# Kernel optimization log

Hardware: AMD Instinct MI355X
Metric: run time of the kernel (lower is better)

## Reference

```python
import jax, jax.numpy as jnp
import numpy as np

N, D, K = 8192, 64, 32

def setup_inputs() -> dict:
    key = jax.random.key(0)
    anchor_x = jax.random.normal(key, (N, D), dtype=jnp.float32)
    return {"anchor_x": anchor_x, "k": K}

def reference(anchor_x, k):
    """Equivalent of NNUtil_GPVAE.build_sequential_nn_idx with faiss/IndexFlatL2.
    For each row r in [k, N), find the k nearest (squared-L2) neighbors among
    rows [0, r) of anchor_x. Returns (sq_dists [N-k, k] ascending, idx [N-k, k]).
    """
    n = anchor_x.shape[0]
    q = anchor_x[k:]                                   # [N-k, D] queries
    sq = jnp.sum(anchor_x * anchor_x, axis=-1)         # [N]
    # squared L2: ||q||^2 + ||x||^2 - 2 q.x  -> [N-k, N]
    dist = sq[k:, None] + sq[None, :] - 2.0 * (q @ anchor_x.T)
    dist = jnp.maximum(dist, 0.0)
    # causal mask: row r may only see database entries j < r (growing index)
    r = jnp.arange(k, n, dtype=jnp.int32)[:, None]     # [N-k, 1]
    j = jnp.arange(n, dtype=jnp.int32)[None, :]        # [1, N]
    dist = jnp.where(j < r, dist, jnp.inf)
    neg_d, idx = jax.lax.top_k(-dist, k)               # ascending distances
    return -neg_d, idx.astype(jnp.int64)
```

## Files before the change

kernel.cpp:

```cpp
#include <hip/hip_runtime.h>
#include <math.h>

#define NROWS 8192
#define DIM   64
#define KSEL  32
#define NQ    (NROWS - KSEL)
#define P1LEN 512
#define CAP   1024
#define FILT_CB 256
#define NMASK (NROWS / 16)

typedef __attribute__((ext_vector_type(8))) short bf16x8;
typedef __attribute__((ext_vector_type(4))) float f32x4;

__global__ void norms_kernel(const float* __restrict__ x, float* __restrict__ sq) {
    int j = blockIdx.x * blockDim.x + threadIdx.x;
    if (j >= NROWS) return;
    const float* xr = x + (size_t)j * DIM;
    float r[8];
#pragma unroll
    for (int u = 0; u < 8; ++u) r[u] = 0.0f;
#pragma unroll
    for (int i = 0; i < DIM; i += 8) {
#pragma unroll
        for (int u = 0; u < 8; ++u)
            r[u] = __fmaf_rn(xr[i + u], xr[i + u], r[u]);
    }
    const float s04 = __fadd_rn(r[0], r[4]);
    const float s26 = __fadd_rn(r[2], r[6]);
    const float s15 = __fadd_rn(r[1], r[5]);
    const float s37 = __fadd_rn(r[3], r[7]);
    sq[j] = __fadd_rn(__fadd_rn(s04, s26), __fadd_rn(s15, s37));
}

__global__ __launch_bounds__(256)
void transpose_kernel(const float* __restrict__ x, float* __restrict__ xT) {
    __shared__ float tile[64][65];
    const int jb  = blockIdx.x * 64;
    const int t   = threadIdx.x;
    const int row = t >> 2;
    const int cb  = (t & 3) * 16;
    const float4* src = reinterpret_cast<const float4*>(
        x + (size_t)(jb + row) * DIM + cb);
#pragma unroll
    for (int i = 0; i < 4; ++i) {
        const float4 v = src[i];
        tile[row][cb + 4 * i + 0] = v.x; tile[row][cb + 4 * i + 1] = v.y;
        tile[row][cb + 4 * i + 2] = v.z; tile[row][cb + 4 * i + 3] = v.w;
    }
    __syncthreads();
    const int k = row;
#pragma unroll
    for (int i = 0; i < 4; ++i) {
        float4 w;
        w.x = tile[cb + 4 * i + 0][k]; w.y = tile[cb + 4 * i + 1][k];
        w.z = tile[cb + 4 * i + 2][k]; w.w = tile[cb + 4 * i + 3][k];
        *reinterpret_cast<float4*>(xT + (size_t)k * NROWS + jb + cb + 4 * i) = w;
    }
}

__global__ __launch_bounds__(256)
void convert_kernel(const float* __restrict__ x, unsigned short* __restrict__ xb) {
    const int i = (blockIdx.x * blockDim.x + threadIdx.x) * 4;
    if (i >= NROWS * DIM) return;
    const float4 v = *reinterpret_cast<const float4*>(x + i);
    const float vv[4] = {v.x, v.y, v.z, v.w};
    unsigned short o[4];
#pragma unroll
    for (int u = 0; u < 4; ++u) {
        const unsigned b = __float_as_uint(vv[u]);
        o[u] = (unsigned short)((b + 0x7FFFu + ((b >> 16) & 1u)) >> 16);
    }
    *reinterpret_cast<ushort4*>(xb + i) = make_ushort4(o[0], o[1], o[2], o[3]);
}

__global__ __launch_bounds__(256)
void pass1_kernel(const float* __restrict__ x, const float* __restrict__ xT,
                  const float* __restrict__ sq,
                  unsigned long long* __restrict__ tau0,
                  unsigned long long* __restrict__ lists) {
    const int wave = threadIdx.x >> 6;
    const int lane = threadIdx.x & 63;
    const int qi   = blockIdx.x * 4 + wave;
    const int r    = qi + KSEL;
    const int P    = min(r, P1LEN);

    const float* qp  = x + (size_t)r * DIM;
    const float  sqr = sq[r];

    float acc[8];
#pragma unroll
    for (int u = 0; u < 8; ++u) acc[u] = 0.0f;
    const float4* xT4 = reinterpret_cast<const float4*>(xT);
#pragma unroll 4
    for (int k = 0; k < DIM; ++k) {
        const float  qk = qp[k];
        const float4 c0 = xT4[(size_t)k * (NROWS / 4) + lane];
        const float4 c1 = xT4[(size_t)k * (NROWS / 4) + 64 + lane];
        acc[0] = __fmaf_rn(qk, c0.x, acc[0]);
        acc[1] = __fmaf_rn(qk, c0.y, acc[1]);
        acc[2] = __fmaf_rn(qk, c0.z, acc[2]);
        acc[3] = __fmaf_rn(qk, c0.w, acc[3]);
        acc[4] = __fmaf_rn(qk, c1.x, acc[4]);
        acc[5] = __fmaf_rn(qk, c1.y, acc[5]);
        acc[6] = __fmaf_rn(qk, c1.z, acc[6]);
        acc[7] = __fmaf_rn(qk, c1.w, acc[7]);
    }

    unsigned long long key[8];
    {
        const float4 sq0 = *reinterpret_cast<const float4*>(sq + 4 * lane);
        const float4 sq1 = *reinterpret_cast<const float4*>(sq + 256 + 4 * lane);
        const float sqc[8] = {sq0.x, sq0.y, sq0.z, sq0.w,
                              sq1.x, sq1.y, sq1.z, sq1.w};
#pragma unroll
        for (int u = 0; u < 8; ++u) {
            const int j = (u < 4) ? (4 * lane + u) : (256 + 4 * lane + (u - 4));
            const float dd = fmaxf(
                __fsub_rn(__fadd_rn(sqr, sqc[u]), __fmul_rn(2.0f, acc[u])), 0.0f);
            key[u] = (j < P)
                ? (((unsigned long long)__float_as_uint(dd) << 32) | (unsigned)j)
                : ~0ull;
        }
    }

    unsigned long long pmin = ~0ull;
#pragma unroll
    for (int s = 0; s < 8; ++s) pmin = key[s] < pmin ? key[s] : pmin;

    unsigned long long g = ~0ull;
    for (int it = 0; it < KSEL; ++it) {
        unsigned long long v = pmin;
#pragma unroll
        for (int off = 32; off > 0; off >>= 1) {
            const unsigned long long o = __shfl_down(v, off, 64);
            v = o < v ? o : v;
        }
        g = __shfl(v, 0, 64);
        if (lane == 0) lists[(size_t)qi * CAP + it] = g;
        if (pmin == g) {
#pragma unroll
            for (int s = 0; s < 8; ++s) if (key[s] == g) key[s] = ~0ull;
            pmin = ~0ull;
#pragma unroll
            for (int s = 0; s < 8; ++s) pmin = key[s] < pmin ? key[s] : pmin;
        }
    }
    if (lane == 0) tau0[qi] = g;
}

__global__ __launch_bounds__(256)
void filter_kernel(const unsigned short* __restrict__ xb,
                   const float* __restrict__ sq,
                   const unsigned long long* __restrict__ tau0,
                   unsigned short* __restrict__ bm) {
    const int qb   = blockIdx.x;
    const int jb   = P1LEN + blockIdx.y * FILT_CB;
    const int r_hi = min(KSEL + (qb + 1) * 64, NROWS);
    if (jb >= r_hi) return;

    const int wave = threadIdx.x >> 6;
    const int lane = threadIdx.x & 63;
    const int rb   = KSEL + qb * 64 + wave * 16;
    const int col  = lane & 15;
    const int kg   = lane >> 4;

    const int arow = min(rb + col, NROWS - 1);
    const bf16x8 a0 = *reinterpret_cast<const bf16x8*>(xb + (size_t)arow * DIM + kg * 8);
    const bf16x8 a1 = *reinterpret_cast<const bf16x8*>(xb + (size_t)arow * DIM + 32 + kg * 8);

    float sqr[4], thm[4]; int rr[4];
#pragma unroll
    for (int i = 0; i < 4; ++i) {
        const int r = rb + kg * 4 + i;
        rr[i]  = r;
        const int rc = min(r, NROWS - 1);
        sqr[i] = sq[rc];
        thm[i] = (r < NROWS) ? __uint_as_float((unsigned)(tau0[r - KSEL] >> 32))
                             : -1.0f;
    }

    for (int sub = 0; sub < FILT_CB / 16; ++sub) {
        const int j0 = jb + sub * 16;
        if (j0 >= r_hi) break;
        const int j  = j0 + col;
        const int jc = min(j, NROWS - 1);
        const bf16x8 b0 = *reinterpret_cast<const bf16x8*>(xb + (size_t)jc * DIM + kg * 8);
        const bf16x8 b1 = *reinterpret_cast<const bf16x8*>(xb + (size_t)jc * DIM + 32 + kg * 8);
        f32x4 acc = {0.f, 0.f, 0.f, 0.f};
        acc = __builtin_amdgcn_mfma_f32_16x16x32_bf16(a0, b0, acc, 0, 0, 0);
        acc = __builtin_amdgcn_mfma_f32_16x16x32_bf16(a1, b1, acc, 0, 0, 0);
        const float sqc = sq[jc];
#pragma unroll
        for (int i = 0; i < 4; ++i) {
            const float s = __fadd_rn(sqr[i], sqc);
            const float d = __fmaf_rn(-2.0f, acc[i], s);
            const bool accept = (j < rr[i]) &&
                                (d <= __fmaf_rn(0.01171875f, s, thm[i]));
            const unsigned long long mask = __ballot(accept);
            const unsigned slice = (unsigned)((mask >> (kg * 16)) & 0xFFFFull);
            if (col == 0 && rr[i] < NROWS)
                bm[(size_t)rr[i] * NMASK + (j0 >> 4)] = (unsigned short)slice;
        }
    }
}

__global__ __launch_bounds__(128)
void refine_merge_kernel(const float* __restrict__ x, const float* __restrict__ sq,
                         const unsigned long long* __restrict__ tau0,
                         const unsigned short* __restrict__ bm,
                         const unsigned long long* __restrict__ lists,
                         float* __restrict__ out_d, float* __restrict__ out_i) {
    __shared__ unsigned long long keys[CAP];
    __shared__ unsigned short jlist[CAP];
    __shared__ unsigned jcnt_s, lcnt;
    const int qi  = blockIdx.x;
    const int r   = qi + KSEL;
    const int tid = threadIdx.x;
    if (tid == 0) { jcnt_s = 0; lcnt = KSEL; }
    if (tid < KSEL) keys[tid] = lists[(size_t)qi * CAP + tid];
    __syncthreads();

    const int mlast = (r - 1) >> 4;
    for (int m = (P1LEN / 16) + tid; m <= mlast; m += 128) {
        unsigned msk = bm[(size_t)r * NMASK + m];
        while (msk) {
            const int b = __builtin_ctz(msk);
            msk &= msk - 1;
            const unsigned slot = atomicAdd(&jcnt_s, 1u);
            if (slot < CAP) jlist[slot] = (unsigned short)((m << 4) + b);
        }
    }
    __syncthreads();

    const unsigned jcnt = min(jcnt_s, (unsigned)CAP);
    const unsigned th = (unsigned)(tau0[qi] >> 32);
    const float* qp = x + (size_t)r * DIM;
    const float  sqr = sq[r];
    for (unsigned idx = tid; idx < jcnt; idx += 128) {
        const int j = (int)jlist[idx];
        const float4* cp4 = reinterpret_cast<const float4*>(x + (size_t)j * DIM);
        float4 c[16];
#pragma unroll
        for (int k = 0; k < 16; ++k) c[k] = cp4[k];
        float acc = 0.0f;
#pragma unroll
        for (int k = 0; k < 16; ++k) {
            acc = __fmaf_rn(qp[4 * k + 0], c[k].x, acc);
            acc = __fmaf_rn(qp[4 * k + 1], c[k].y, acc);
            acc = __fmaf_rn(qp[4 * k + 2], c[k].z, acc);
            acc = __fmaf_rn(qp[4 * k + 3], c[k].w, acc);
        }
        const float dd = fmaxf(
            __fsub_rn(__fadd_rn(sqr, sq[j]), __fmul_rn(2.0f, acc)), 0.0f);
        const unsigned bits = __float_as_uint(dd);
        if (bits <= th) {
            const unsigned slot = atomicAdd(&lcnt, 1u);
            if (slot < CAP)
                keys[slot] = ((unsigned long long)bits << 32) | (unsigned)j;
        }
    }
    __syncthreads();

    if (tid >= 64) return;
    const int lane = tid;
    const int ne   = min((int)lcnt, CAP);

    unsigned long long k[16];
#pragma unroll
    for (int s = 0; s < 16; ++s) {
        const int idx = lane + (s << 6);
        k[s] = (idx < ne) ? keys[idx] : ~0ull;
    }
    unsigned long long pmin = ~0ull;
#pragma unroll
    for (int s = 0; s < 16; ++s) pmin = k[s] < pmin ? k[s] : pmin;

    for (int it = 0; it < KSEL; ++it) {
        unsigned long long v = pmin;
#pragma unroll
        for (int off = 32; off > 0; off >>= 1) {
            const unsigned long long o = __shfl_down(v, off, 64);
            v = o < v ? o : v;
        }
        const unsigned long long g = __shfl(v, 0, 64);
        if (lane == 0) {
            out_d[(size_t)qi * KSEL + it] = __uint_as_float((unsigned)(g >> 32));
            out_i[(size_t)qi * KSEL + it] = (float)(unsigned)(g & 0xFFFFFFFFu);
        }
        if (pmin == g) {
#pragma unroll
            for (int s = 0; s < 16; ++s) if (k[s] == g) k[s] = ~0ull;
            pmin = ~0ull;
#pragma unroll
            for (int s = 0; s < 16; ++s) pmin = k[s] < pmin ? k[s] : pmin;
        }
    }
}

extern "C" void kernel_launch(void* const* d_in, const int* in_sizes, int n_in,
                              void* d_out, int out_size, void* d_ws, size_t ws_size,
                              hipStream_t stream) {
    const float* x = (const float*)d_in[0];
    float* sq = (float*)d_ws;
    unsigned long long* tau0 =
        (unsigned long long*)((char*)d_ws + 32768);
    unsigned long long* lists =
        (unsigned long long*)((char*)d_ws + 131072);
    unsigned short* xb =
        (unsigned short*)((char*)d_ws + 66977792);
    float* xT = (float*)((char*)d_ws + 68026368);
    unsigned short* bm =
        (unsigned short*)((char*)d_ws + 70123520);
    float* out_d = (float*)d_out;
    float* out_i = out_d + (size_t)NQ * KSEL;

    norms_kernel<<<NROWS / 256, 256, 0, stream>>>(x, sq);
    transpose_kernel<<<NROWS / 64, 256, 0, stream>>>(x, xT);
    convert_kernel<<<NROWS * DIM / 1024, 256, 0, stream>>>(x, xb);
    pass1_kernel<<<NQ / 4, 256, 0, stream>>>(x, xT, sq, tau0, lists);
    dim3 gf(128, (NROWS - P1LEN) / FILT_CB);
    filter_kernel<<<gf, 256, 0, stream>>>(xb, sq, tau0, bm);
    refine_merge_kernel<<<NQ, 128, 0, stream>>>(x, sq, tau0, bm, lists,
                                                out_d, out_i);
}
```

Before: 284.4 us.

## Use wave-aggregated atomics and two-wave split top-k in refine-merge kernel

The mask-expansion phase now loads four mask words per thread and uses a wave prefix scan with a single atomic per wave, replacing one LDS atomic per set bit. The candidate append path likewise uses ballot plus a leader atomic, and the per-row float4 register array is streamed rather than fully preloaded. The final top-32 selection is split so both waves each extract a partial top-32 from half the keys, and then one wave merges the 64 candidates. This is meant to cut LDS atomic contention and shorten the serial selection loop. It adds an extra barrier and a shuffle-heavy merge step.

```diff
diff --git a/kernel.cpp b/kernel.cpp
--- a/kernel.cpp
+++ b/kernel.cpp
@@ -212,23 +212,48 @@
                          const unsigned long long* __restrict__ lists,
                          float* __restrict__ out_d, float* __restrict__ out_i) {
     __shared__ unsigned long long keys[CAP];
+    __shared__ unsigned long long semi[2 * KSEL];
     __shared__ unsigned short jlist[CAP];
     __shared__ unsigned jcnt_s, lcnt;
     const int qi  = blockIdx.x;
     const int r   = qi + KSEL;
     const int tid = threadIdx.x;
+    const int ln  = tid & 63;
     if (tid == 0) { jcnt_s = 0; lcnt = KSEL; }
     if (tid < KSEL) keys[tid] = lists[(size_t)qi * CAP + tid];
     __syncthreads();
 
     const int mlast = (r - 1) >> 4;
-    for (int m = (P1LEN / 16) + tid; m <= mlast; m += 128) {
-        unsigned msk = bm[(size_t)r * NMASK + m];
-        while (msk) {
-            const int b = __builtin_ctz(msk);
-            msk &= msk - 1;
-            const unsigned slot = atomicAdd(&jcnt_s, 1u);
-            if (slot < CAP) jlist[slot] = (unsigned short)((m << 4) + b);
+    unsigned ww[4];
+#pragma unroll
+    for (int s = 0; s < 4; ++s) {
+        const int m = (P1LEN / 16) + tid + s * 128;
+        ww[s] = (m <= mlast) ? (unsigned)bm[(size_t)r * NMASK + m] : 0u;
+    }
+    {
+        const unsigned cnt = (unsigned)(__popc(ww[0]) + __popc(ww[1]) +
+                                        __popc(ww[2]) + __popc(ww[3]));
+        unsigned pre = cnt;
+#pragma unroll
+        for (int off = 1; off < 64; off <<= 1) {
+            const unsigned o = __shfl_up(pre, off, 64);
+            if (ln >= off) pre += o;
+        }
+        const unsigned total = __shfl(pre, 63, 64);
+        unsigned base = 0;
+        if (ln == 63 && total) base = atomicAdd(&jcnt_s, total);
+        base = __shfl(base, 63, 64);
+        unsigned pos = base + pre - cnt;
+#pragma unroll
+        for (int s = 0; s < 4; ++s) {
+            unsigned msk = ww[s];
+            const int m = (P1LEN / 16) + tid + s * 128;
+            while (msk) {
+                const int b = __builtin_ctz(msk);
+                msk &= msk - 1;
+                if (pos < CAP) jlist[pos] = (unsigned short)((m << 4) + b);
+                ++pos;
+            }
         }
     }
     __syncthreads();
@@ -237,64 +262,90 @@
     const unsigned th = (unsigned)(tau0[qi] >> 32);
     const float* qp = x + (size_t)r * DIM;
     const float  sqr = sq[r];
-    for (unsigned idx = tid; idx < jcnt; idx += 128) {
-        const int j = (int)jlist[idx];
+    const int rounds = (int)((jcnt + 127) >> 7);
+    for (int rd = 0; rd < rounds; ++rd) {
+        const unsigned idx = (unsigned)rd * 128 + (unsigned)tid;
+        const bool valid = (idx < jcnt);
+        const int j = valid ? (int)jlist[idx] : 0;
         const float4* cp4 = reinterpret_cast<const float4*>(x + (size_t)j * DIM);
-        float4 c[16];
-#pragma unroll
-        for (int k = 0; k < 16; ++k) c[k] = cp4[k];
         float acc = 0.0f;
 #pragma unroll
         for (int k = 0; k < 16; ++k) {
-            acc = __fmaf_rn(qp[4 * k + 0], c[k].x, acc);
-            acc = __fmaf_rn(qp[4 * k + 1], c[k].y, acc);
-            acc = __fmaf_rn(qp[4 * k + 2], c[k].z, acc);
-            acc = __fmaf_rn(qp[4 * k + 3], c[k].w, acc);
+            const float4 c = cp4[k];
+            acc = __fmaf_rn(qp[4 * k + 0], c.x, acc);
+            acc = __fmaf_rn(qp[4 * k + 1], c.y, acc);
+            acc = __fmaf_rn(qp[4 * k + 2], c.z, acc);
+            acc = __fmaf_rn(qp[4 * k + 3], c.w, acc);
         }
         const float dd = fmaxf(
             __fsub_rn(__fadd_rn(sqr, sq[j]), __fmul_rn(2.0f, acc)), 0.0f);
         const unsigned bits = __float_as_uint(dd);
-        if (bits <= th) {
-            const unsigned slot = atomicAdd(&lcnt, 1u);
-            if (slot < CAP)
-                keys[slot] = ((unsigned long long)bits << 32) | (unsigned)j;
+        const bool keep = valid && (bits <= th);
+        const unsigned long long mask = __ballot(keep);
+        if (mask) {
+            const int leader = __builtin_ctzll(mask);
+            unsigned base = 0;
+            if (ln == leader)
+                base = atomicAdd(&lcnt, (unsigned)__popcll(mask));
+            base = __shfl(base, leader, 64);
+            if (keep) {
+                const unsigned slot =
+                    base + (unsigned)__popcll(mask & ((1ull << ln) - 1ull));
+                if (slot < CAP)
+                    keys[slot] = ((unsigned long long)bits << 32) | (unsigned)j;
+            }
+        }
+    }
+    __syncthreads();
+
+    const int ne = min((int)lcnt, CAP);
+    {
+        const int wv = tid >> 6;
+        unsigned long long k[8];
+#pragma unroll
+        for (int s = 0; s < 8; ++s) {
+            const int i2 = wv * 64 + ln + s * 128;
+            k[s] = (i2 < ne) ? keys[i2] : ~0ull;
+        }
+        unsigned long long pmin = ~0ull;
+#pragma unroll
+        for (int s = 0; s < 8; ++s) pmin = k[s] < pmin ? k[s] : pmin;
+
+        for (int it = 0; it < KSEL; ++it) {
+            unsigned long long v = pmin;
+#pragma unroll
+            for (int off = 32; off > 0; off >>= 1) {
+                const unsigned long long o = __shfl_down(v, off, 64);
+                v = o < v ? o : v;
+            }
+            const unsigned long long g = __shfl(v, 0, 64);
+            if (ln == 0) semi[wv * KSEL + it] = g;
+            if (pmin == g) {
+#pragma unroll
+                for (int s = 0; s < 8; ++s) if (k[s] == g) k[s] = ~0ull;
+                pmin = ~0ull;
+#pragma unroll
+                for (int s = 0; s < 8; ++s) pmin = k[s] < pmin ? k[s] : pmin;
+            }
         }
     }
     __syncthreads();
 
     if (tid >= 64) return;
-    const int lane = tid;
-    const int ne   = min((int)lcnt, CAP);
-
-    unsigned long long k[16];
-#pragma unroll
-    for (int s = 0; s < 16; ++s) {
-        const int idx = lane + (s << 6);
-        k[s] = (idx < ne) ? keys[idx] : ~0ull;
-    }
-    unsigned long long pmin = ~0ull;
-#pragma unroll
-    for (int s = 0; s < 16; ++s) pmin = k[s] < pmin ? k[s] : pmin;
-
+    unsigned long long kk = semi[tid];
     for (int it = 0; it < KSEL; ++it) {
-        unsigned long long v = pmin;
+        unsigned long long v = kk;
 #pragma unroll
         for (int off = 32; off > 0; off >>= 1) {
             const unsigned long long o = __shfl_down(v, off, 64);
             v = o < v ? o : v;
         }
         const unsigned long long g = __shfl(v, 0, 64);
-        if (lane == 0) {
+        if (tid == 0) {
             out_d[(size_t)qi * KSEL + it] = __uint_as_float((unsigned)(g >> 32));
             out_i[(size_t)qi * KSEL + it] = (float)(unsigned)(g & 0xFFFFFFFFu);
         }
-        if (pmin == g) {
-#pragma unroll
-            for (int s = 0; s < 16; ++s) if (k[s] == g) k[s] = ~0ull;
-            pmin = ~0ull;
-#pragma unroll
-            for (int s = 0; s < 16; ++s) pmin = k[s] < pmin ? k[s] : pmin;
-        }
+        if (kk == g) kk = ~0ull;
     }
 }
 
```

Result: slower. 444.3 us (+56.2%).
